# Optimization experiments

Measured on AMD Instinct MI355X. Metric: run time of the kernel, lower is better.

Reference implementation:

```python
import jax, jax.numpy as jnp
import numpy as np

B, L, E, H = 8, 2048, 768, 512

def setup_inputs() -> dict:
    key = jax.random.key(0)
    ks = jax.random.split(key, 12)
    s = 0.05
    rn = lambda k, shp: jax.random.normal(k, shp, dtype=jnp.float32) * s
    return {
        "embedded_inputs": jax.random.normal(ks[0], (B, L, E), dtype=jnp.float32),
        "decoder_input_init": jax.random.normal(ks[1], (B, H), dtype=jnp.float32),
        "W_ih": rn(ks[2], (4 * H, E)), "W_hh": rn(ks[3], (4 * H, H)),
        "b_ih": jnp.zeros((4 * H,), jnp.float32), "b_hh": jnp.zeros((4 * H,), jnp.float32),
        "Wd_in": rn(ks[4], (4 * H, H)), "bd_in": jnp.zeros((4 * H,), jnp.float32),
        "Wd_hh": rn(ks[5], (4 * H, H)), "bd_hh": jnp.zeros((4 * H,), jnp.float32),
        "W_inp": rn(ks[6], (H, H)), "b_inp": jnp.zeros((H,), jnp.float32),
        "Wc": rn(ks[7], (H, H)), "bc": jnp.zeros((H,), jnp.float32),
        "V": jax.random.uniform(ks[8], (H,), minval=-1.0, maxval=1.0, dtype=jnp.float32),
        "W_out": rn(ks[9], (H, 2 * H)), "b_out": jnp.zeros((H,), jnp.float32),
    }


def _lstm_cell(x, h, c, W_in, b_in, W_hid, b_hid):
    # gates chunked in (input, forget, cell, out) order, matching torch .chunk(4,1)
    g = x @ W_in.T + b_in + h @ W_hid.T + b_hid
    i, f, gc, o = jnp.split(g, 4, axis=-1)
    c_t = jax.nn.sigmoid(f) * c + jax.nn.sigmoid(i) * jnp.tanh(gc)
    h_t = jax.nn.sigmoid(o) * jnp.tanh(c_t)
    return h_t, c_t


def _encode(x, W_ih, W_hh, b_ih, b_hh):
    # x: [B, L, E] -> outputs [B, L, H], last (h, c)
    Hh = W_hh.shape[1]
    h0 = jnp.zeros((x.shape[0], Hh), x.dtype)
    def step(carry, xt):
        h, c = carry
        h, c = _lstm_cell(xt, h, c, W_ih, b_ih, W_hh, b_hh)
        return (h, c), h
    (hT, cT), outs = jax.lax.scan(step, (h0, h0), x.transpose(1, 0, 2))
    return outs.transpose(1, 0, 2), hT, cT


def reference(embedded_inputs, decoder_input_init, W_ih, W_hh, b_ih, b_hh,
              Wd_in, bd_in, Wd_hh, bd_hh, W_inp, b_inp, Wc, bc, V, W_out, b_out):
    enc_out, h, c = _encode(embedded_inputs, W_ih, W_hh, b_ih, b_hh)  # [B,L,H]
    context = enc_out
    Bc, Lc = context.shape[0], context.shape[1]
    # Conv1d(k=1) over permuted context == per-position linear -> ctx [B,H,L]
    ctx = jnp.einsum('blh,oh->bol', context, Wc) + bc[None, :, None]
    mask = jnp.ones((Bc, Lc), context.dtype)
    x = decoder_input_init
    outputs, pointers = [], []
    for _ in range(2):  # source decodes exactly 2 pointers (start/end)
        h_t, c = _lstm_cell(x, h, c, Wd_in, bd_in, Wd_hh, bd_hh)
        inp = (h_t @ W_inp.T + b_inp)[:, :, None]                 # [B,H,1]
        att = jnp.einsum('h,bhl->bl', V, jnp.tanh(inp + ctx))     # [B,L]
        att = jnp.where(mask == 0, -jnp.inf, att)
        alpha = jax.nn.softmax(att, axis=1)
        hidden_state = jnp.einsum('bhl,bl->bh', ctx, alpha)
        h = jnp.tanh(jnp.concatenate([hidden_state, h_t], axis=-1) @ W_out.T + b_out)
        idx = jnp.argmax(alpha * mask, axis=1)
        onehot = jax.nn.one_hot(idx, Lc, dtype=mask.dtype)
        mask = mask * (1.0 - onehot)
        x = jnp.take_along_axis(enc_out, idx[:, None, None], axis=1)[:, 0, :]
        outputs.append(alpha)
        pointers.append(idx)
    return jnp.stack(outputs, axis=1), jnp.stack(pointers, axis=1)
```

## Files before the change

kernel.cpp:

```cpp
#include <hip/hip_runtime.h>
#include <math.h>

#define B_   8
#define L_   2048
#define E_   768
#define H_   512
#define G4_  2048
#define CL_  512

static __device__ __forceinline__ float sigm(float x){ return 1.0f/(1.0f+expf(-x)); }
static __device__ __forceinline__ float ftanh(float x){
  float ax = fabsf(x);
  float e  = expf(2.0f*ax);
  float r  = 1.0f - 2.0f/(e+1.0f);
  return copysignf(r, x);
}

__device__ __forceinline__ void gemm_body(
    const float* __restrict__ A, const float* __restrict__ W,
    const float* __restrict__ bias1, const float* __restrict__ bias2,
    float* __restrict__ C, int N, int K, int CL, int Ltot, int c0,
    int CLc, int Ltotc, int c0c, int bm, int bn)
{
  __shared__ float As[16][132];
  __shared__ float Bs[16][132];
  const int tid = threadIdx.x;

  const int r  = tid >> 1;
  const int kq = (tid & 1) * 8;
  const int am = bm + r;
  const int ab = am / CL, al = am % CL;
  const float* Arow = A + ((size_t)ab * Ltot + c0 + al) * K;
  const float* Wrow = W + (size_t)(bn + r) * K;

  const int tx = tid & 15, ty = tid >> 4;
  float acc[8][8] = {};

  for (int k0 = 0; k0 < K; k0 += 16) {
    float4 a0 = *(const float4*)(Arow + k0 + kq);
    float4 a1 = *(const float4*)(Arow + k0 + kq + 4);
    float4 w0 = *(const float4*)(Wrow + k0 + kq);
    float4 w1 = *(const float4*)(Wrow + k0 + kq + 4);
    __syncthreads();
    As[kq+0][r]=a0.x; As[kq+1][r]=a0.y; As[kq+2][r]=a0.z; As[kq+3][r]=a0.w;
    As[kq+4][r]=a1.x; As[kq+5][r]=a1.y; As[kq+6][r]=a1.z; As[kq+7][r]=a1.w;
    Bs[kq+0][r]=w0.x; Bs[kq+1][r]=w0.y; Bs[kq+2][r]=w0.z; Bs[kq+3][r]=w0.w;
    Bs[kq+4][r]=w1.x; Bs[kq+5][r]=w1.y; Bs[kq+6][r]=w1.z; Bs[kq+7][r]=w1.w;
    __syncthreads();
    #pragma unroll
    for (int k = 0; k < 16; ++k) {
      float4 x0 = *(const float4*)&As[k][ty*4];
      float4 x1 = *(const float4*)&As[k][64 + ty*4];
      float4 y0 = *(const float4*)&Bs[k][tx*4];
      float4 y1 = *(const float4*)&Bs[k][64 + tx*4];
      float av[8] = {x0.x,x0.y,x0.z,x0.w, x1.x,x1.y,x1.z,x1.w};
      float bv[8] = {y0.x,y0.y,y0.z,y0.w, y1.x,y1.y,y1.z,y1.w};
      #pragma unroll
      for (int i=0;i<8;++i)
        #pragma unroll
        for (int j=0;j<8;++j)
          acc[i][j] += av[i]*bv[j];
    }
  }

  float bs[8];
  #pragma unroll
  for (int j=0;j<4;++j) {
    int c0n = bn + tx*4 + j, c1n = bn + 64 + tx*4 + j;
    bs[j]   = bias1[c0n] + (bias2 ? bias2[c0n] : 0.0f);
    bs[4+j] = bias1[c1n] + (bias2 ? bias2[c1n] : 0.0f);
  }
  #pragma unroll
  for (int i=0;i<8;++i) {
    int r0 = bm + ((i<4) ? (ty*4+i) : (64 + ty*4 + (i-4)));
    int cb = r0 / CLc, cl = r0 % CLc;
    size_t crow = (size_t)cb * Ltotc + c0c + cl;
    float4 o0 = { acc[i][0]+bs[0], acc[i][1]+bs[1], acc[i][2]+bs[2], acc[i][3]+bs[3] };
    float4 o1 = { acc[i][4]+bs[4], acc[i][5]+bs[5], acc[i][6]+bs[6], acc[i][7]+bs[7] };
    *(float4*)&C[crow*N + bn + tx*4]      = o0;
    *(float4*)&C[crow*N + bn + 64 + tx*4] = o1;
  }
}

__global__ __launch_bounds__(256) void gemm128(
    const float* __restrict__ A, const float* __restrict__ W,
    const float* __restrict__ bias1, const float* __restrict__ bias2,
    float* __restrict__ C, int N, int K, int CL, int Ltot, int c0,
    int CLc, int Ltotc, int c0c)
{
  gemm_body(A, W, bias1, bias2, C, N, K, CL, Ltot, c0, CLc, Ltotc, c0c,
            blockIdx.y*128, blockIdx.x*128);
}

__device__ __forceinline__ void recur_body(
    const float* __restrict__ Xp, const float* __restrict__ Whh,
    float* __restrict__ enc_out, unsigned long long* __restrict__ hb2,
    float* __restrict__ cbuf, float* __restrict__ hT, int t0, int nsteps)
{
  const int tid = threadIdx.x;
  const int b   = blockIdx.x >> 5;
  const int m   = blockIdx.x & 31;
  const int c   = tid >> 4;
  const int q   = tid & 15;
  const int j   = m*16 + c;

  __shared__ float hsh[2][512];
  __shared__ float xpsh[2][64];

  float4 w4[4][8];
  #pragma unroll
  for (int gi = 0; gi < 4; ++gi) {
    const float* wr = Whh + ((size_t)(gi*H_ + j))*H_ + q*4;
    #pragma unroll
    for (int k = 0; k < 8; ++k) w4[gi][k] = *(const float4*)(wr + k*64);
  }
  float cc = 0.0f;
  if (q == 0) cc = cbuf[b*H_ + j];

  float xv = 0.0f;
  if (tid < 64)
    xv = Xp[((size_t)(b*CL_ + 0))*G4_ + (size_t)(tid>>4)*H_ + m*16 + (tid&15)];

  const bool own = ((tid >> 3) == m);

  for (int s = 0; s < nsteps; ++s) {
    const int t = t0 + s;
    const int p = s & 1;

    if (tid < 64) {
      xpsh[p][tid] = xv;
      if (s + 1 < nsteps)
        xv = Xp[((size_t)(b*CL_ + s + 1))*G4_ + (size_t)(tid>>4)*H_ + m*16 + (tid&15)];
    }

    if (!(own && s > 0)) {
      const unsigned long long* src =
          hb2 + ((size_t)(t & 1))*(B_*H_) + (size_t)b*H_ + tid*2;
      unsigned long long v0 = 0, v1 = 0;
      bool d0 = false, d1 = false;
      do {
        if (!d0) v0 = __hip_atomic_load(src,   __ATOMIC_RELAXED, __HIP_MEMORY_SCOPE_AGENT);
        if (!d1) v1 = __hip_atomic_load(src+1, __ATOMIC_RELAXED, __HIP_MEMORY_SCOPE_AGENT);
        d0 = d0 || ((unsigned)(v0 >> 32) == (unsigned)t);
        d1 = d1 || ((unsigned)(v1 >> 32) == (unsigned)t);
      } while (!(d0 && d1));
      union { unsigned u; float f; } a0u, a1u;
      a0u.u = (unsigned)v0; a1u.u = (unsigned)v1;
      hsh[p][2*tid]   = a0u.f;
      hsh[p][2*tid+1] = a1u.f;
    }
    __syncthreads();

    float xg0=0.f, xg1=0.f, xg2=0.f, xg3=0.f;
    if (q == 0) {
      xg0 = xpsh[p][c];      xg1 = xpsh[p][16+c];
      xg2 = xpsh[p][32+c];   xg3 = xpsh[p][48+c];
    }

    float a0=0.f, a1=0.f, a2=0.f, a3=0.f;
    #pragma unroll
    for (int k = 0; k < 8; ++k) {
      float4 h4 = *(const float4*)&hsh[p][q*4 + k*64];
      a0 = fmaf(w4[0][k].x,h4.x, fmaf(w4[0][k].y,h4.y, fmaf(w4[0][k].z,h4.z, fmaf(w4[0][k].w,h4.w, a0))));
      a1 = fmaf(w4[1][k].x,h4.x, fmaf(w4[1][k].y,h4.y, fmaf(w4[1][k].z,h4.z, fmaf(w4[1][k].w,h4.w, a1))));
      a2 = fmaf(w4[2][k].x,h4.x, fmaf(w4[2][k].y,h4.y, fmaf(w4[2][k].z,h4.z, fmaf(w4[2][k].w,h4.w, a2))));
      a3 = fmaf(w4[3][k].x,h4.x, fmaf(w4[3][k].y,h4.y, fmaf(w4[3][k].z,h4.z, fmaf(w4[3][k].w,h4.w, a3))));
    }
    #pragma unroll
    for (int msk = 1; msk < 16; msk <<= 1) {
      a0 += __shfl_xor(a0, msk, 64);
      a1 += __shfl_xor(a1, msk, 64);
      a2 += __shfl_xor(a2, msk, 64);
      a3 += __shfl_xor(a3, msk, 64);
    }

    if (q == 0) {
      float g0 = a0 + xg0, g1 = a1 + xg1, g2 = a2 + xg2, g3 = a3 + xg3;
      cc = sigm(g1)*cc + sigm(g0)*ftanh(g2);
      float hn = sigm(g3)*ftanh(cc);
      union { float f; unsigned u; } hu; hu.f = hn;
      unsigned long long wv =
          (((unsigned long long)(unsigned)(t + 1)) << 32) | (unsigned long long)hu.u;
      __hip_atomic_store(hb2 + ((size_t)((t+1) & 1))*(B_*H_) + (size_t)b*H_ + j, wv,
                         __ATOMIC_RELAXED, __HIP_MEMORY_SCOPE_AGENT);
      hsh[p^1][j] = hn;
      enc_out[((size_t)b*L_ + t)*H_ + j] = hn;
      if (t == L_ - 1) hT[b*H_ + j] = hn;
    }
  }
  if (q == 0) cbuf[b*H_ + j] = cc;
}

__global__ __launch_bounds__(256, 1) void fused_rg(
    const float* __restrict__ Xp, const float* __restrict__ Whh,
    float* __restrict__ enc_out, unsigned long long* __restrict__ hb2,
    float* __restrict__ cbuf, float* __restrict__ hT, int t0, int nsteps,
    const float* __restrict__ A, const float* __restrict__ W,
    const float* __restrict__ bias1, const float* __restrict__ bias2,
    float* __restrict__ C, int gN, int gK, int gCL, int gLtot, int gc0,
    int gCLc, int gLtotc, int gc0c, int gbx)
{
  if ((int)blockIdx.x < 256) {
    recur_body(Xp, Whh, enc_out, hb2, cbuf, hT, t0, nsteps);
  } else {
    const int b2 = (int)blockIdx.x - 256;
    gemm_body(A, W, bias1, bias2, C, gN, gK, gCL, gLtot, gc0,
              gCLc, gLtotc, gc0c, (b2 / gbx) * 128, (b2 % gbx) * 128);
  }
}

__global__ __launch_bounds__(256) void dual_mv(
    const float* __restrict__ x1, const float* __restrict__ W1, int ld1, int K1,
    const float* __restrict__ x2, const float* __restrict__ W2, int ld2, int K2,
    const float* __restrict__ bias1, const float* __restrict__ bias2,
    float* __restrict__ out, int N, int act)
{
  const int w = blockIdx.x*4 + (threadIdx.x>>6);
  const int lane = threadIdx.x & 63;
  const int b = w / N, n = w % N;
  float s = 0.0f;
  for (int k = lane*4; k < K1; k += 256) {
    float4 xv = *(const float4*)(x1 + (size_t)b*K1 + k);
    float4 wv = *(const float4*)(W1 + (size_t)n*ld1 + k);
    s += xv.x*wv.x + xv.y*wv.y + xv.z*wv.z + xv.w*wv.w;
  }
  if (x2) {
    for (int k = lane*4; k < K2; k += 256) {
      float4 xv = *(const float4*)(x2 + (size_t)b*K2 + k);
      float4 wv = *(const float4*)(W2 + (size_t)n*ld2 + k);
      s += xv.x*wv.x + xv.y*wv.y + xv.z*wv.z + xv.w*wv.w;
    }
  }
  #pragma unroll
  for (int m=32; m>0; m>>=1) s += __shfl_xor(s, m, 64);
  if (lane == 0) {
    float r = s + bias1[n] + (bias2 ? bias2[n] : 0.0f);
    if (act) r = tanhf(r);
    out[(size_t)b*N + n] = r;
  }
}

__global__ void dec_cell(const float* __restrict__ g, float* __restrict__ c,
                         float* __restrict__ ht)
{
  int i = blockIdx.x*256 + threadIdx.x;
  int b = i >> 9, j = i & 511;
  const float* gb = g + (size_t)b*G4_;
  float gi_ = gb[j], gf = gb[H_+j], gg = gb[2*H_+j], go = gb[3*H_+j];
  float cc = c[i];
  cc = sigm(gf)*cc + sigm(gi_)*tanhf(gg);
  ht[i] = sigm(go)*tanhf(cc);
  c[i]  = cc;
}

__global__ __launch_bounds__(256) void dec_att(
    const float* __restrict__ inp, const float* __restrict__ ctx,
    const float* __restrict__ V, float* __restrict__ att)
{
  const int w = blockIdx.x*4 + (threadIdx.x>>6);
  const int lane = threadIdx.x & 63;
  const int b = w >> 11;
  const float* cr = ctx + (size_t)w*H_;
  const float* ip = inp + (size_t)b*H_;
  float s = 0.0f;
  #pragma unroll
  for (int i=0;i<2;++i) {
    int k = lane*4 + i*256;
    float4 c4 = *(const float4*)(cr+k);
    float4 i4 = *(const float4*)(ip+k);
    float4 v4 = *(const float4*)(V+k);
    s += v4.x*tanhf(i4.x+c4.x) + v4.y*tanhf(i4.y+c4.y)
       + v4.z*tanhf(i4.z+c4.z) + v4.w*tanhf(i4.w+c4.w);
  }
  #pragma unroll
  for (int m=32; m>0; m>>=1) s += __shfl_xor(s, m, 64);
  if (lane == 0) att[w] = s;
}

__global__ __launch_bounds__(256) void dec_softmax(
    const float* __restrict__ att, const float* __restrict__ enc,
    int iter, int* __restrict__ chosen,
    float* __restrict__ out_alpha, float* __restrict__ out_ptr,
    float* __restrict__ x_next)
{
  const int b = blockIdx.x, tid = threadIdx.x;
  __shared__ float rv[256]; __shared__ int ri[256];
  __shared__ float s_mx, s_sum; __shared__ int s_idx;
  const int banned = iter ? chosen[b] : -1;
  float a[8]; float mx = -INFINITY;
  #pragma unroll
  for (int i=0;i<8;++i) {
    int l = (i<<8)+tid;
    float v = att[(size_t)b*L_ + l];
    if (l == banned) v = -INFINITY;
    a[i] = v; mx = fmaxf(mx, v);
  }
  rv[tid]=mx; __syncthreads();
  for (int s=128;s>0;s>>=1){ if (tid<s) rv[tid]=fmaxf(rv[tid],rv[tid+s]); __syncthreads(); }
  if (tid==0) s_mx = rv[0];
  __syncthreads();
  const float MX = s_mx;
  __syncthreads();
  float sum = 0.0f;
  #pragma unroll
  for (int i=0;i<8;++i) {
    int l = (i<<8)+tid;
    float pexp = (l == banned) ? 0.0f : expf(a[i]-MX);
    sum += pexp; a[i] = pexp;
  }
  rv[tid]=sum; __syncthreads();
  for (int s=128;s>0;s>>=1){ if (tid<s) rv[tid]+=rv[tid+s]; __syncthreads(); }
  if (tid==0) s_sum = rv[0];
  __syncthreads();
  const float inv = 1.0f/s_sum;
  __syncthreads();
  float vb = -1.0f; int ib = 1<<30;
  #pragma unroll
  for (int i=0;i<8;++i) {
    int l = (i<<8)+tid;
    if (l != banned) { float v = a[i]; if (v > vb || (v == vb && l < ib)) { vb=v; ib=l; } }
  }
  rv[tid]=vb; ri[tid]=ib; __syncthreads();
  for (int s=128;s>0;s>>=1) {
    if (tid<s) {
      float v2=rv[tid+s]; int i2=ri[tid+s];
      if (v2 > rv[tid] || (v2 == rv[tid] && i2 < ri[tid])) { rv[tid]=v2; ri[tid]=i2; }
    }
    __syncthreads();
  }
  if (tid==0) {
    s_idx = ri[0];
    out_ptr[b*2+iter] = (float)ri[0];
    if (iter==0) chosen[b] = ri[0];
  }
  __syncthreads();
  #pragma unroll
  for (int i=0;i<8;++i) {
    int l = (i<<8)+tid;
    out_alpha[((size_t)b*2+iter)*L_ + l] = a[i]*inv;
  }
  const int idx = s_idx;
  for (int j=tid; j<H_; j+=256)
    x_next[(size_t)b*H_ + j] = enc[((size_t)b*L_ + idx)*H_ + j];
}

__global__ void dec_hidden1(const float* __restrict__ ctx, const float* __restrict__ alpha_all,
                            int iter, float* __restrict__ part)
{
  const int b = blockIdx.x >> 4, ch = blockIdx.x & 15;
  const int j = threadIdx.x;
  const float* al = alpha_all + ((size_t)b*2+iter)*L_ + ch*128;
  const float* cp = ctx + ((size_t)b*L_ + ch*128)*H_ + j;
  float s = 0.0f;
  for (int l=0; l<128; ++l) s += cp[(size_t)l*H_] * al[l];
  part[((size_t)b*16+ch)*H_ + j] = s;
}

__global__ void dec_hidden2(const float* __restrict__ part, float* __restrict__ hid)
{
  int i = blockIdx.x*256 + threadIdx.x;
  int b = i >> 9, j = i & 511;
  float s = 0.0f;
  #pragma unroll
  for (int ch=0; ch<16; ++ch) s += part[((size_t)b*16+ch)*H_ + j];
  hid[i] = s;
}

extern "C" void kernel_launch(void* const* d_in, const int* in_sizes, int n_in,
                              void* d_out, int out_size, void* d_ws, size_t ws_size,
                              hipStream_t stream)
{
  const float* emb   = (const float*)d_in[0];
  const float* x0    = (const float*)d_in[1];
  const float* W_ih  = (const float*)d_in[2];
  const float* W_hh  = (const float*)d_in[3];
  const float* b_ih  = (const float*)d_in[4];
  const float* b_hh  = (const float*)d_in[5];
  const float* Wd_in = (const float*)d_in[6];
  const float* bd_in = (const float*)d_in[7];
  const float* Wd_hh = (const float*)d_in[8];
  const float* bd_hh = (const float*)d_in[9];
  const float* W_inp = (const float*)d_in[10];
  const float* b_inp = (const float*)d_in[11];
  const float* Wc    = (const float*)d_in[12];
  const float* bc    = (const float*)d_in[13];
  const float* V     = (const float*)d_in[14];
  const float* W_out = (const float*)d_in[15];
  const float* b_out = (const float*)d_in[16];

  const size_t BIG = 8388608;
  const size_t tail_floats = 8192*2  + 4096 + 4096 + 16384 + 4096*4 + 16384 + 65536 + 64;
  const bool dbuf = ws_size >= (3*BIG + tail_floats) * sizeof(float);

  float* ws  = (float*)d_ws;
  float* XPA = ws;
  float* XPB = dbuf ? (XPA + BIG) : XPA;
  float* ENC = (dbuf ? XPB : XPA) + BIG;
  unsigned long long* HB2 = (unsigned long long*)(ENC + BIG);
  float* HB  = (float*)(HB2 + 8192);
  float* CB  = HB + 4096;
  float* DG  = CB + 4096;
  float* HT  = DG + 16384;
  float* INP = HT + 4096;
  float* ATT = INP + 4096;
  float* HID = ATT + 16384;
  float* XN  = HID + 4096;
  float* HD  = XN + 4096;
  float* PART = HD + 4096;
  int* CHOSEN = (int*)(PART + 65536);
  float* CTX = XPA;

  hipMemsetAsync(HB2, 0, 8192*sizeof(unsigned long long) + (4096+4096)*sizeof(float), stream);

  if (dbuf) {
    gemm128<<<dim3(G4_/128, (B_*CL_)/128), 256, 0, stream>>>(
        emb, W_ih, b_ih, b_hh, XPA, G4_, E_, CL_, L_, 0*CL_, 1<<30, 0, 0);
    float* xpsrc = XPA; float* xpdst = XPB;
    for (int c = 0; c < 3; ++c) {
      fused_rg<<<256 + 512, 256, 0, stream>>>(
          xpsrc, W_hh, ENC, HB2, CB, HB, c*CL_, CL_,
          emb, W_ih, b_ih, b_hh, xpdst, G4_, E_, CL_, L_, (c+1)*CL_,
          1<<30, 0, 0, 16);
      float* tmp = xpsrc; xpsrc = xpdst; xpdst = tmp;
    }
    fused_rg<<<256 + 384, 256, 0, stream>>>(
        xpsrc, W_hh, ENC, HB2, CB, HB, 3*CL_, CL_,
        ENC, Wc, bc, nullptr, CTX, H_, H_, 1536, L_, 0,
        1536, L_, 0, 4);
    gemm128<<<dim3(H_/128, (B_*CL_)/128), 256, 0, stream>>>(
        ENC, Wc, bc, nullptr, CTX, H_, H_, CL_, L_, 1536, CL_, L_, 1536);
  } else {
    for (int c = 0; c < 4; ++c) {
      gemm128<<<dim3(G4_/128, (B_*CL_)/128), 256, 0, stream>>>(
          emb, W_ih, b_ih, b_hh, XPA, G4_, E_, CL_, L_, c*CL_, 1<<30, 0, 0);
      fused_rg<<<256, 256, 0, stream>>>(
          XPA, W_hh, ENC, HB2, CB, HB, c*CL_, CL_,
          nullptr, nullptr, nullptr, nullptr, nullptr, 0, 0, 1, 1, 0, 1, 1, 0, 1);
    }
    gemm128<<<dim3(H_/128, (B_*L_)/128), 256, 0, stream>>>(
        ENC, Wc, bc, nullptr, CTX, H_, H_, L_, L_, 0, 1<<30, 0, 0);
  }

  float* out = (float*)d_out;
  const float* x_cur = x0;
  const float* h_cur = HB;
  for (int iter=0; iter<2; ++iter) {
    dual_mv<<<(B_*G4_)/4, 256, 0, stream>>>(x_cur, Wd_in, H_, H_,
                                            h_cur, Wd_hh, H_, H_,
                                            bd_in, bd_hh, DG, G4_, 0);
    dec_cell<<<16, 256, 0, stream>>>(DG, CB, HT);
    dual_mv<<<(B_*H_)/4, 256, 0, stream>>>(HT, W_inp, H_, H_,
                                           nullptr, nullptr, 0, 0,
                                           b_inp, nullptr, INP, H_, 0);
    dec_att<<<(B_*L_)/4, 256, 0, stream>>>(INP, CTX, V, ATT);
    dec_softmax<<<B_, 256, 0, stream>>>(ATT, ENC, iter, CHOSEN, out, out + 32768, XN);
    dec_hidden1<<<B_*16, 512, 0, stream>>>(CTX, out, iter, PART);
    dec_hidden2<<<16, 256, 0, stream>>>(PART, HID);
    dual_mv<<<(B_*H_)/4, 256, 0, stream>>>(HID, W_out, 2*H_, H_,
                                           HT, W_out + H_, 2*H_, H_,
                                           b_out, nullptr, HD, H_, 1);
    x_cur = XN; h_cur = HD;
  }
}
```

Baseline: 4.871 ms.

## Split recurrent matvec across waves by K-slice and reduce partials in shared memory

```diff
diff --git a/kernel.cpp b/kernel.cpp
--- a/kernel.cpp
+++ b/kernel.cpp
@@ -97,43 +97,38 @@
     float* __restrict__ enc_out, unsigned long long* __restrict__ hb2,
     float* __restrict__ cbuf, float* __restrict__ hT, int t0, int nsteps)
 {
-  const int tid = threadIdx.x;
-  const int b   = blockIdx.x >> 5;
-  const int m   = blockIdx.x & 31;
-  const int c   = tid >> 4;
-  const int q   = tid & 15;
-  const int j   = m*16 + c;
-
-  __shared__ float hsh[2][512];
-  __shared__ float xpsh[2][64];
-
-  float4 w4[4][8];
-  #pragma unroll
-  for (int gi = 0; gi < 4; ++gi) {
-    const float* wr = Whh + ((size_t)(gi*H_ + j))*H_ + q*4;
-    #pragma unroll
-    for (int k = 0; k < 8; ++k) w4[gi][k] = *(const float4*)(wr + k*64);
-  }
+  const int tid  = threadIdx.x;
+  const int w    = tid >> 6;
+  const int lane = tid & 63;
+  const int b    = blockIdx.x >> 5;
+  const int m    = blockIdx.x & 31;
+  const int j0   = m*16;
+  const int g    = lane >> 4;
+  const int r    = lane & 15;
+
+  __shared__ float hws[4][128];
+  __shared__ float part[2][4][64];
+
+  const bool isAct = (lane < 4);
+  const int  ai    = w*4 + lane;
+  const int  aj    = j0 + ai;
+
   float cc = 0.0f;
-  if (q == 0) cc = cbuf[b*H_ + j];
-
-  float xv = 0.0f;
-  if (tid < 64)
-    xv = Xp[((size_t)(b*CL_ + 0))*G4_ + (size_t)(tid>>4)*H_ + m*16 + (tid&15)];
-
-  const bool own = ((tid >> 3) == m);
+  float xn0=0.f, xn1=0.f, xn2=0.f, xn3=0.f;
+  if (isAct) {
+    cc = cbuf[b*H_ + aj];
+    const float* xp = Xp + ((size_t)(b*CL_ + 0))*G4_ + aj;
+    xn0 = xp[0]; xn1 = xp[H_]; xn2 = xp[2*H_]; xn3 = xp[3*H_];
+  }
+
+  const float* wrow = Whh + ((size_t)(g*H_ + j0 + r))*H_ + 128*w;
 
   for (int s = 0; s < nsteps; ++s) {
     const int t = t0 + s;
+    const unsigned ut = (unsigned)t;
     const int p = s & 1;
 
-    if (tid < 64) {
-      xpsh[p][tid] = xv;
-      if (s + 1 < nsteps)
-        xv = Xp[((size_t)(b*CL_ + s + 1))*G4_ + (size_t)(tid>>4)*H_ + m*16 + (tid&15)];
-    }
-
-    if (!(own && s > 0)) {
+    {
       const unsigned long long* src =
           hb2 + ((size_t)(t & 1))*(B_*H_) + (size_t)b*H_ + tid*2;
       unsigned long long v0 = 0, v1 = 0;
@@ -141,54 +136,57 @@
       do {
         if (!d0) v0 = __hip_atomic_load(src,   __ATOMIC_RELAXED, __HIP_MEMORY_SCOPE_AGENT);
         if (!d1) v1 = __hip_atomic_load(src+1, __ATOMIC_RELAXED, __HIP_MEMORY_SCOPE_AGENT);
-        d0 = d0 || ((unsigned)(v0 >> 32) == (unsigned)t);
-        d1 = d1 || ((unsigned)(v1 >> 32) == (unsigned)t);
+        d0 = d0 || ((unsigned)(v0 >> 32) == ut);
+        d1 = d1 || ((unsigned)(v1 >> 32) == ut);
       } while (!(d0 && d1));
-      union { unsigned u; float f; } a0u, a1u;
-      a0u.u = (unsigned)v0; a1u.u = (unsigned)v1;
-      hsh[p][2*tid]   = a0u.f;
-      hsh[p][2*tid+1] = a1u.f;
-    }
-    __syncthreads();
-
-    float xg0=0.f, xg1=0.f, xg2=0.f, xg3=0.f;
-    if (q == 0) {
-      xg0 = xpsh[p][c];      xg1 = xpsh[p][16+c];
-      xg2 = xpsh[p][32+c];   xg3 = xpsh[p][48+c];
-    }
+      union { unsigned u; float f; } u0, u1;
+      u0.u = (unsigned)v0; u1.u = (unsigned)v1;
+      hws[w][2*lane]   = u0.f;
+      hws[w][2*lane+1] = u1.f;
+    }
+    __builtin_amdgcn_wave_barrier();
 
     float a0=0.f, a1=0.f, a2=0.f, a3=0.f;
     #pragma unroll
     for (int k = 0; k < 8; ++k) {
-      float4 h4 = *(const float4*)&hsh[p][q*4 + k*64];
-      a0 = fmaf(w4[0][k].x,h4.x, fmaf(w4[0][k].y,h4.y, fmaf(w4[0][k].z,h4.z, fmaf(w4[0][k].w,h4.w, a0))));
-      a1 = fmaf(w4[1][k].x,h4.x, fmaf(w4[1][k].y,h4.y, fmaf(w4[1][k].z,h4.z, fmaf(w4[1][k].w,h4.w, a1))));
-      a2 = fmaf(w4[2][k].x,h4.x, fmaf(w4[2][k].y,h4.y, fmaf(w4[2][k].z,h4.z, fmaf(w4[2][k].w,h4.w, a2))));
-      a3 = fmaf(w4[3][k].x,h4.x, fmaf(w4[3][k].y,h4.y, fmaf(w4[3][k].z,h4.z, fmaf(w4[3][k].w,h4.w, a3))));
-    }
-    #pragma unroll
-    for (int msk = 1; msk < 16; msk <<= 1) {
-      a0 += __shfl_xor(a0, msk, 64);
-      a1 += __shfl_xor(a1, msk, 64);
-      a2 += __shfl_xor(a2, msk, 64);
-      a3 += __shfl_xor(a3, msk, 64);
-    }
-
-    if (q == 0) {
-      float g0 = a0 + xg0, g1 = a1 + xg1, g2 = a2 + xg2, g3 = a3 + xg3;
+      float4 h0 = ((const float4*)hws[w])[4*k+0];
+      float4 h1 = ((const float4*)hws[w])[4*k+1];
+      float4 h2 = ((const float4*)hws[w])[4*k+2];
+      float4 h3 = ((const float4*)hws[w])[4*k+3];
+      float4 w0 = ((const float4*)wrow)[4*k+0];
+      float4 w1 = ((const float4*)wrow)[4*k+1];
+      float4 w2 = ((const float4*)wrow)[4*k+2];
+      float4 w3 = ((const float4*)wrow)[4*k+3];
+      a0 = fmaf(w0.x,h0.x, fmaf(w0.y,h0.y, fmaf(w0.z,h0.z, fmaf(w0.w,h0.w, a0))));
+      a1 = fmaf(w1.x,h1.x, fmaf(w1.y,h1.y, fmaf(w1.z,h1.z, fmaf(w1.w,h1.w, a1))));
+      a2 = fmaf(w2.x,h2.x, fmaf(w2.y,h2.y, fmaf(w2.z,h2.z, fmaf(w2.w,h2.w, a2))));
+      a3 = fmaf(w3.x,h3.x, fmaf(w3.y,h3.y, fmaf(w3.z,h3.z, fmaf(w3.w,h3.w, a3))));
+    }
+    part[p][w][lane] = (a0+a1) + (a2+a3);
+    __syncthreads();
+
+    if (isAct) {
+      float G0 = part[p][0][ 0+ai] + part[p][1][ 0+ai] + part[p][2][ 0+ai] + part[p][3][ 0+ai];
+      float G1 = part[p][0][16+ai] + part[p][1][16+ai] + part[p][2][16+ai] + part[p][3][16+ai];
+      float G2 = part[p][0][32+ai] + part[p][1][32+ai] + part[p][2][32+ai] + part[p][3][32+ai];
+      float G3 = part[p][0][48+ai] + part[p][1][48+ai] + part[p][2][48+ai] + part[p][3][48+ai];
+      float g0 = G0 + xn0, g1 = G1 + xn1, g2 = G2 + xn2, g3 = G3 + xn3;
       cc = sigm(g1)*cc + sigm(g0)*ftanh(g2);
       float hn = sigm(g3)*ftanh(cc);
       union { float f; unsigned u; } hu; hu.f = hn;
       unsigned long long wv =
-          (((unsigned long long)(unsigned)(t + 1)) << 32) | (unsigned long long)hu.u;
-      __hip_atomic_store(hb2 + ((size_t)((t+1) & 1))*(B_*H_) + (size_t)b*H_ + j, wv,
+          (((unsigned long long)(ut + 1u)) << 32) | (unsigned long long)hu.u;
+      __hip_atomic_store(hb2 + ((size_t)((t+1) & 1))*(B_*H_) + (size_t)b*H_ + aj, wv,
                          __ATOMIC_RELAXED, __HIP_MEMORY_SCOPE_AGENT);
-      hsh[p^1][j] = hn;
-      enc_out[((size_t)b*L_ + t)*H_ + j] = hn;
-      if (t == L_ - 1) hT[b*H_ + j] = hn;
-    }
-  }
-  if (q == 0) cbuf[b*H_ + j] = cc;
+      enc_out[((size_t)b*L_ + t)*H_ + aj] = hn;
+      if (t == L_ - 1) hT[b*H_ + aj] = hn;
+      if (s + 1 < nsteps) {
+        const float* xp = Xp + ((size_t)(b*CL_ + s + 1))*G4_ + aj;
+        xn0 = xp[0]; xn1 = xp[H_]; xn2 = xp[2*H_]; xn3 = xp[3*H_];
+      }
+    }
+  }
+  if (isAct) cbuf[b*H_ + aj] = cc;
 }
 
 __global__ __launch_bounds__(256, 1) void fused_rg(
```

Measured after the change: 5.288 ms. +8.6%, slower.
